# Optimization experiments

Measured on AMD Instinct MI355X. Metric: run time of the kernel, lower is better.

The kernel has to match this reference:

```python
import jax, jax.numpy as jnp
import numpy as np

DIM = 25
N_NODES = 20000
N_EDGES = 320000
NFEAT = 300
NHID = 64
NCLASS = 50


def setup_inputs() -> dict:
    key = jax.random.key(0)
    ks = jax.random.split(key, 8)
    s1 = np.sqrt(6.0 / (NFEAT + NHID))
    s2 = np.sqrt(6.0 / (NHID * DIM + NCLASS))
    return {
        "x": jax.random.normal(ks[0], (N_NODES, NFEAT), dtype=jnp.float32),
        "adj_rows": jax.random.randint(ks[1], (DIM, N_EDGES), 0, N_NODES, dtype=jnp.int32),
        "adj_cols": jax.random.randint(ks[2], (DIM, N_EDGES), 0, N_NODES, dtype=jnp.int32),
        "adj_vals": jax.random.uniform(ks[3], (DIM, N_EDGES), dtype=jnp.float32),
        "W1": jax.random.uniform(ks[4], (DIM, NFEAT, NHID), dtype=jnp.float32, minval=-s1, maxval=s1),
        "b1": jnp.zeros((DIM, NHID), dtype=jnp.float32),
        "W2": jax.random.uniform(ks[5], (DIM, NHID * DIM, NCLASS), dtype=jnp.float32, minval=-s2, maxval=s2),
        "b2": jnp.zeros((DIM, NCLASS), dtype=jnp.float32),
    }


def _spmm(rows, cols, vals, sup, n):
    # sparse [n,n] @ dense [n,f] via gather + segment-sum scatter-add
    return jax.ops.segment_sum(vals[:, None] * sup[cols], rows, num_segments=n)


def reference(x, adj_rows, adj_cols, adj_vals, W1, b1, W2, b2):
    n = x.shape[0]
    spmm = jax.vmap(lambda r, c, v, s: _spmm(r, c, v, s, n))
    # layer 1: per-branch dense mm, spmm, bias, relu  -> [DIM, n, NHID]
    sup1 = jnp.einsum("nf,dfh->dnh", x, W1)
    h1 = jax.nn.relu(spmm(adj_rows, adj_cols, adj_vals, sup1) + b1[:, None, :])
    # permute + reshape: concat branch features per node -> [n, DIM*NHID]
    h1cat = jnp.transpose(h1, (1, 0, 2)).reshape(n, -1)
    # layer 2: per-branch dense mm, spmm, bias, relu -> [DIM, n, NCLASS]
    sup2 = jnp.einsum("nk,dkc->dnc", h1cat, W2)
    h2 = jax.nn.relu(spmm(adj_rows, adj_cols, adj_vals, sup2) + b2[:, None, :])
    # max-pool over branches (POOLING='max')
    return jnp.max(h2, axis=0)
```

## Files before the change

kernel.cpp:

```cpp
#include <hip/hip_runtime.h>
#include <hip/hip_bf16.h>
#include <cstdint>
#include <cstddef>

#define DIM 25
#define NN 20000
#define NE 320000
#define NF 300
#define NH 64
#define NC 50
#define K2 (DIM*NH)
#define KP1 320
#define B1T_ROWS 1664
#define B2T_ROWS 1280
#define NBK 79
#define EPB 4096
#define BPB ((NE + EPB - 1) / EPB)
#define FCAP 5632

typedef __attribute__((ext_vector_type(8))) short short8;
typedef __attribute__((ext_vector_type(4))) float floatx4;
typedef __hip_bfloat16 bf16;

static __device__ __forceinline__ unsigned bf16bits(float f) {
    bf16 b = __float2bfloat16(f);
    return (unsigned)*reinterpret_cast<unsigned short*>(&b);
}
static __device__ __forceinline__ float blo(unsigned w) { return __uint_as_float(w << 16); }
static __device__ __forceinline__ float bhi(unsigned w) { return __uint_as_float(w & 0xFFFF0000u); }

static __device__ __forceinline__ void gld16(const void* g, void* l) {
    __builtin_amdgcn_global_load_lds((const __attribute__((address_space(1))) unsigned*)g,
                                     (__attribute__((address_space(3))) unsigned*)l, 16, 0, 0);
}

__global__ void zero_kernel(int* __restrict__ p, int n) {
    int i = blockIdx.x * blockDim.x + threadIdx.x;
    if (i < n) p[i] = 0;
}

__global__ __launch_bounds__(256) void bucket_scatter_kernel(const int* __restrict__ rows,
                                                             const int* __restrict__ cols,
                                                             const float* __restrict__ vals,
                                                             int* __restrict__ gcur,
                                                             unsigned* __restrict__ interE,
                                                             unsigned char* __restrict__ interR) {
    const int d = blockIdx.y;
    const int e0 = blockIdx.x * EPB;
    __shared__ int lh[NBK];
    __shared__ int lo[NBK];
    __shared__ int lbase[NBK];
    __shared__ unsigned entE[EPB];
    __shared__ unsigned short entR[EPB];
    const int tid = threadIdx.x;
    for (int i = tid; i < NBK; i += 256) lh[i] = 0;
    __syncthreads();
    const int* rd = rows + (size_t)d * NE;
    const int* cd = cols + (size_t)d * NE;
    const float* vd = vals + (size_t)d * NE;
    const int e1 = min(e0 + EPB, NE);
    const int ne = e1 - e0;
    for (int i = e0 + tid; i < e1; i += 256)
        atomicAdd(&lh[rd[i] >> 8], 1);
    __syncthreads();
    if (tid == 0) {
        int run = 0;
        for (int b = 0; b < NBK; ++b) { lo[b] = run; run += lh[b]; }
    }
    __syncthreads();
    for (int i = tid; i < NBK; i += 256) {
        lbase[i] = lh[i] ? atomicAdd(&gcur[d * NBK + i], lh[i]) : 0;
        lh[i] = 0;
    }
    __syncthreads();
    for (int i = e0 + tid; i < e1; i += 256) {
        int r = rd[i];
        int b = r >> 8;
        int rank = atomicAdd(&lh[b], 1);
        int pos = lo[b] + rank;
        entE[pos] = (unsigned)cd[i] | (bf16bits(vd[i]) << 16);
        entR[pos] = (unsigned short)r;
    }
    __syncthreads();
    for (int p = tid; p < ne; p += 256) {
        int r = entR[p];
        int b = r >> 8;
        int gpos = lbase[b] + (p - lo[b]);
        if (gpos < FCAP) {
            size_t slot = ((size_t)d * NBK + b) * FCAP + gpos;
            interE[slot] = entE[p];
            interR[slot] = (unsigned char)r;
        }
    }
}

__global__ void bucket_scan_kernel(const int* __restrict__ gcur,
                                   int* __restrict__ offs_b,
                                   int* __restrict__ bcnt,
                                   int* __restrict__ offs) {
    const int d = blockIdx.x;
    if (threadIdx.x != 0) return;
    int run = 0;
    for (int b = 0; b < NBK; ++b) {
        int c = min(gcur[d * NBK + b], FCAP);
        offs_b[d * NBK + b] = run;
        bcnt[d * NBK + b] = c;
        run += c;
    }
    offs[d * (NN + 1) + NN] = run;
}

__global__ __launch_bounds__(256) void csr_finalize_kernel(const unsigned* __restrict__ interE,
                                                           const unsigned char* __restrict__ interR,
                                                           const int* __restrict__ offs_b,
                                                           const int* __restrict__ bcnt,
                                                           int* __restrict__ offs,
                                                           unsigned* __restrict__ sedge) {
    const int d = blockIdx.y;
    const int b = blockIdx.x;
    const int tid = threadIdx.x;
    const int s = offs_b[d * NBK + b];
    const int cnt = bcnt[d * NBK + b];
    const size_t base = ((size_t)d * NBK + b) * FCAP;
    __shared__ int sm[256];
    __shared__ int cur[256];
    __shared__ unsigned lse[FCAP];
    sm[tid] = 0;
    __syncthreads();
    for (int i = tid; i < cnt; i += 256)
        atomicAdd(&sm[interR[base + i]], 1);
    __syncthreads();
    int own = sm[tid];
    for (int off = 1; off < 256; off <<= 1) {
        int t = (tid >= off) ? sm[tid - off] : 0;
        __syncthreads();
        sm[tid] += t;
        __syncthreads();
    }
    int excl = sm[tid] - own;
    int row = (b << 8) + tid;
    if (row < NN) offs[d * (NN + 1) + row] = s + excl;
    cur[tid] = excl;
    __syncthreads();
    for (int i = tid; i < cnt; i += 256) {
        int idx = atomicAdd(&cur[interR[base + i]], 1);
        lse[idx] = interE[base + i];
    }
    __syncthreads();
    unsigned* sed = sedge + (size_t)d * NE;
    for (int t = tid; t < cnt; t += 256)
        sed[s + t] = lse[t];
}

__global__ void pack_x_kernel(const float* __restrict__ x, bf16* __restrict__ xb) {
    int i = blockIdx.x * blockDim.x + threadIdx.x;
    if (i >= NN * KP1) return;
    int n = i / KP1, k = i - n * KP1;
    xb[i] = __float2bfloat16((k < NF) ? x[(size_t)n * NF + k] : 0.f);
}

__global__ void pack_b1_kernel(const float* __restrict__ W1, bf16* __restrict__ b1t) {
    int i = blockIdx.x * blockDim.x + threadIdx.x;
    if (i >= B1T_ROWS * KP1) return;
    int j2 = i / KP1, k = i - j2 * KP1;
    int chunk = j2 >> 9;
    int r = j2 & 511;
    int d = chunk * 8 + (r >> 6);
    float v = 0.f;
    if (d < DIM && k < NF)
        v = W1[(size_t)d * NF * NH + (size_t)k * NH + (r & 63)];
    b1t[i] = __float2bfloat16(v);
}

__global__ void pack_b2_kernel(const float* __restrict__ W2, bf16* __restrict__ b2t) {
    int i = blockIdx.x * blockDim.x + threadIdx.x;
    if (i >= B2T_ROWS * K2) return;
    int r = i / K2, k = i - r * K2;
    float v = 0.f;
    if (r < DIM * NC) {
        int g = r / NC, c = r - g * NC;
        v = W2[(size_t)g * K2 * NC + (size_t)k * NC + c];
    }
    b2t[i] = __float2bfloat16(v);
}

__global__ __launch_bounds__(256) void gemm_bf16_kernel(const bf16* __restrict__ A, int lda,
                                                        const bf16* __restrict__ BT, int ldb,
                                                        bf16* __restrict__ C,
                                                        int ksteps, int mode, int nvalid) {
    __shared__ unsigned short As[2 * 128 * 32];
    __shared__ unsigned short Bs[2 * 128 * 32];
    const int tid = threadIdx.x;
    const int wave = tid >> 6;
    const int lane = tid & 63;

    const int mtiles = (int)gridDim.x;
    const int ntiles = (int)gridDim.y;
    const int bid = (int)blockIdx.y * mtiles + (int)blockIdx.x;
    const int per_group = 8 * ntiles;
    const int group = bid / per_group;
    const int rem = bid - group * per_group;
    const int first_m = group * 8;
    const int gm = min(8, mtiles - first_m);
    const int mt = first_m + rem % gm;
    const int nt = rem / gm;
    const int m0 = mt * 128;
    const int n0 = nt * 128;

    const int wm = (wave >> 1) * 64;
    const int wn = (wave & 1) * 64;
    floatx4 acc[4][4] = {};
    const int r0 = tid >> 2;
    const int cg = (tid & 3) ^ ((r0 >> 1) & 3);
    const int q8 = (lane >> 4) * 8;
    const int gq = q8 >> 3;
    unsigned short* lA0 = As + wave * 512;
    unsigned short* lA1 = As + 2048 + wave * 512;
    unsigned short* lB0 = Bs + wave * 512;
    unsigned short* lB1 = Bs + 2048 + wave * 512;
    const bf16* gA0 = A + (size_t)(m0 + r0) * lda + cg * 8;
    const bf16* gA1 = A + (size_t)(m0 + r0 + 64) * lda + cg * 8;
    const bf16* gB0 = BT + (size_t)(n0 + r0) * ldb + cg * 8;
    const bf16* gB1 = BT + (size_t)(n0 + r0 + 64) * ldb + cg * 8;

    int offA[4], offB[4];
    #pragma unroll
    for (int i = 0; i < 4; ++i) {
        int ra = wm + i * 16 + (lane & 15);
        int rb = wn + i * 16 + (lane & 15);
        offA[i] = ra * 32 + ((gq ^ ((ra >> 1) & 3)) << 3);
        offB[i] = rb * 32 + ((gq ^ ((rb >> 1) & 3)) << 3);
    }

    gld16(gA0, lA0); gld16(gA1, lA1); gld16(gB0, lB0); gld16(gB1, lB1);
    __syncthreads();

    int cur = 0;
    for (int ks = 0; ks < ksteps; ++ks) {
        if (ks + 1 < ksteps) {
            const int nb = cur ^ 1;
            const size_t ko = (size_t)(ks + 1) * 32;
            gld16(gA0 + ko, lA0 + nb * 4096); gld16(gA1 + ko, lA1 + nb * 4096);
            gld16(gB0 + ko, lB0 + nb * 4096); gld16(gB1 + ko, lB1 + nb * 4096);
        }
        const unsigned short* as = As + cur * 4096;
        const unsigned short* bs = Bs + cur * 4096;
        short8 af[4], bfr[4];
        #pragma unroll
        for (int i = 0; i < 4; ++i) {
            af[i]  = *(const short8*)&as[offA[i]];
            bfr[i] = *(const short8*)&bs[offB[i]];
        }
        #pragma unroll
        for (int i = 0; i < 4; ++i)
            #pragma unroll
            for (int j = 0; j < 4; ++j)
                acc[i][j] = __builtin_amdgcn_mfma_f32_16x16x32_bf16(af[i], bfr[j], acc[i][j], 0, 0, 0);
        __syncthreads();
        cur ^= 1;
    }
    const int cr = (lane >> 4) * 4;
    const int cc = lane & 15;
    #pragma unroll
    for (int i = 0; i < 4; ++i) {
        #pragma unroll
        for (int r = 0; r < 4; ++r) {
            int m = m0 + wm + i * 16 + cr + r;
            if (m >= NN) continue;
            #pragma unroll
            for (int j = 0; j < 4; ++j) {
                int n = n0 + wn + j * 16 + cc;
                if (n >= nvalid) continue;
                if (mode == 1) {
                    int g = n >> 6, h = n & 63;
                    C[(size_t)g * NN * NH + (size_t)m * NH + h] = __float2bfloat16(acc[i][j][r]);
                } else {
                    int g = n / NC, c = n - g * NC;
                    C[(size_t)g * NN * NC + (size_t)m * NC + c] = __float2bfloat16(acc[i][j][r]);
                }
            }
        }
    }
}

__global__ __launch_bounds__(256) void spmm1_kernel(const bf16* __restrict__ sup,
                                                    const int* __restrict__ offs,
                                                    const unsigned* __restrict__ sedge,
                                                    const float* __restrict__ b1,
                                                    bf16* __restrict__ h1cat, int d0, int CHk) {
    const int i = blockIdx.x;
    const int g = i % CHk;
    const int nb = i / CHk;
    const int tid = threadIdx.x;
    const int lane = tid & 63;
    const int n = nb * 8 + ((tid >> 6) << 1) + (lane >> 5);
    const int hl = lane & 31;
    const int d = d0 + g;
    const int s = offs[d * (NN + 1) + n];
    const int e = offs[d * (NN + 1) + n + 1];
    const char* supd = (const char*)sup + (size_t)g * NN * NH * 2;
    const unsigned* sed = sedge + (size_t)d * NE;
    const unsigned hoff = (unsigned)hl * 4;
    float alo0 = 0.f, ahi0 = 0.f, alo1 = 0.f, ahi1 = 0.f;
    int j = s;
    for (; j + 4 <= e; j += 4) {
        unsigned e0 = sed[j], e1 = sed[j + 1], e2 = sed[j + 2], e3 = sed[j + 3];
        unsigned w0 = *(const unsigned*)(supd + (((e0 & 0xFFFFu) << 7) | hoff));
        unsigned w1 = *(const unsigned*)(supd + (((e1 & 0xFFFFu) << 7) | hoff));
        unsigned w2 = *(const unsigned*)(supd + (((e2 & 0xFFFFu) << 7) | hoff));
        unsigned w3 = *(const unsigned*)(supd + (((e3 & 0xFFFFu) << 7) | hoff));
        float v0 = bhi(e0), v1 = bhi(e1), v2 = bhi(e2), v3 = bhi(e3);
        alo0 = fmaf(v0, blo(w0), alo0); ahi0 = fmaf(v0, bhi(w0), ahi0);
        alo1 = fmaf(v1, blo(w1), alo1); ahi1 = fmaf(v1, bhi(w1), ahi1);
        alo0 = fmaf(v2, blo(w2), alo0); ahi0 = fmaf(v2, bhi(w2), ahi0);
        alo1 = fmaf(v3, blo(w3), alo1); ahi1 = fmaf(v3, bhi(w3), ahi1);
    }
    for (; j < e; ++j) {
        unsigned e0 = sed[j];
        unsigned w0 = *(const unsigned*)(supd + (((e0 & 0xFFFFu) << 7) | hoff));
        float v0 = bhi(e0);
        alo0 = fmaf(v0, blo(w0), alo0); ahi0 = fmaf(v0, bhi(w0), ahi0);
    }
    float alo = fmaxf((alo0 + alo1) + b1[d * NH + 2 * hl], 0.f);
    float ahi = fmaxf((ahi0 + ahi1) + b1[d * NH + 2 * hl + 1], 0.f);
    unsigned packed = bf16bits(alo) | (bf16bits(ahi) << 16);
    *(unsigned*)((char*)h1cat + ((size_t)n * K2 + d * NH) * 2 + hoff) = packed;
}

__global__ __launch_bounds__(256) void spmm2b_kernel(const bf16* __restrict__ sup2,
                                                     const int* __restrict__ offs,
                                                     const unsigned* __restrict__ sedge,
                                                     const float* __restrict__ b2,
                                                     unsigned* __restrict__ h2u) {
    const int i = blockIdx.x;
    const int r = i & 7;
    const int q = i >> 3;
    int d, nb;
    if (q < 7500) { d = r + 8 * (q / 2500); nb = q % 2500; }
    else { d = 24; nb = (q - 7500) * 8 + r; if (nb >= 2500) return; }
    const int tid = threadIdx.x;
    const int lane = tid & 63;
    const int n = nb * 8 + ((tid >> 6) << 1) + (lane >> 5);
    const int cl = min(lane & 31, 24);
    const unsigned coff = (unsigned)cl * 4;
    const int s = offs[d * (NN + 1) + n];
    const int e = offs[d * (NN + 1) + n + 1];
    const char* supd = (const char*)sup2 + (size_t)d * NN * NC * 2;
    const unsigned* sed = sedge + (size_t)d * NE;
    float alo0 = b2[d * NC + 2 * cl], ahi0 = b2[d * NC + 2 * cl + 1];
    float alo1 = 0.f, ahi1 = 0.f;
    int j = s;
    for (; j + 4 <= e; j += 4) {
        unsigned e0 = sed[j], e1 = sed[j + 1], e2 = sed[j + 2], e3 = sed[j + 3];
        unsigned w0 = *(const unsigned*)(supd + ((e0 & 0xFFFFu) * 100u + coff));
        unsigned w1 = *(const unsigned*)(supd + ((e1 & 0xFFFFu) * 100u + coff));
        unsigned w2 = *(const unsigned*)(supd + ((e2 & 0xFFFFu) * 100u + coff));
        unsigned w3 = *(const unsigned*)(supd + ((e3 & 0xFFFFu) * 100u + coff));
        float v0 = bhi(e0), v1 = bhi(e1), v2 = bhi(e2), v3 = bhi(e3);
        alo0 = fmaf(v0, blo(w0), alo0); ahi0 = fmaf(v0, bhi(w0), ahi0);
        alo1 = fmaf(v1, blo(w1), alo1); ahi1 = fmaf(v1, bhi(w1), ahi1);
        alo0 = fmaf(v2, blo(w2), alo0); ahi0 = fmaf(v2, bhi(w2), ahi0);
        alo1 = fmaf(v3, blo(w3), alo1); ahi1 = fmaf(v3, bhi(w3), ahi1);
    }
    for (; j < e; ++j) {
        unsigned e0 = sed[j];
        unsigned w0 = *(const unsigned*)(supd + ((e0 & 0xFFFFu) * 100u + coff));
        float v0 = bhi(e0);
        alo0 = fmaf(v0, blo(w0), alo0); ahi0 = fmaf(v0, bhi(w0), ahi0);
    }
    float alo = fmaxf(alo0 + alo1, 0.f);
    float ahi = fmaxf(ahi0 + ahi1, 0.f);
    if ((lane & 31) < 25)
        h2u[((size_t)d * NN + n) * 25 + cl] = bf16bits(alo) | (bf16bits(ahi) << 16);
}

__global__ __launch_bounds__(256) void maxk_kernel(const unsigned* __restrict__ h2u,
                                                   float* __restrict__ out) {
    int i = blockIdx.x * blockDim.x + threadIdx.x;
    if (i >= NN * 25) return;
    int n = i / 25, cl = i - n * 25;
    float mlo = 0.f, mhi = 0.f;
    #pragma unroll
    for (int d = 0; d < DIM; ++d) {
        unsigned w = h2u[(size_t)d * NN * 25 + i];
        mlo = fmaxf(mlo, blo(w));
        mhi = fmaxf(mhi, bhi(w));
    }
    *(float2*)&out[(size_t)n * NC + 2 * cl] = make_float2(mlo, mhi);
}

extern "C" void kernel_launch(void* const* d_in, const int* in_sizes, int n_in,
                              void* d_out, int out_size, void* d_ws, size_t ws_size,
                              hipStream_t stream) {
    const float* x    = (const float*)d_in[0];
    const int*   rows = (const int*)d_in[1];
    const int*   cols = (const int*)d_in[2];
    const float* vals = (const float*)d_in[3];
    const float* W1   = (const float*)d_in[4];
    const float* b1   = (const float*)d_in[5];
    const float* W2   = (const float*)d_in[6];
    const float* b2   = (const float*)d_in[7];
    float* out = (float*)d_out;

    char* ws = (char*)d_ws;
    size_t off = 0;
    auto alloc = [&](size_t bytes) {
        void* p = ws + off;
        off += (bytes + 255) & ~(size_t)255;
        return p;
    };
    bf16* supbuf = (bf16*)alloc(sizeof(bf16) * (size_t)DIM * NN * NC);
    bf16* h1cat  = (bf16*)alloc(sizeof(bf16) * (size_t)NN * K2);
    bf16* b1t    = (bf16*)alloc(sizeof(bf16) * (size_t)B1T_ROWS * KP1);
    bf16* b2t    = (bf16*)alloc(sizeof(bf16) * (size_t)B2T_ROWS * K2);
    int*  offs   = (int*)alloc(sizeof(int) * (size_t)DIM * (NN + 1));
    int*  gcur   = (int*)alloc(sizeof(int) * (size_t)DIM * NBK);
    int*  offs_b = (int*)alloc(sizeof(int) * (size_t)DIM * NBK);
    int*  bcnt   = (int*)alloc(sizeof(int) * (size_t)DIM * NBK);
    unsigned* sedge = (unsigned*)alloc(sizeof(unsigned) * (size_t)DIM * NE);

    bf16* sup1 = supbuf;
    bf16* xbf  = supbuf + (size_t)12 * 1024 * 1024;
    bf16* sup2 = supbuf;
    unsigned* interE = (unsigned*)h1cat;
    unsigned char* interR = (unsigned char*)h1cat + (size_t)DIM * NBK * FCAP * 4;
    unsigned* h2u = (unsigned*)h1cat;

    if (off > ws_size) return;

    zero_kernel<<<(DIM * NBK + 255) / 256, 256, 0, stream>>>(gcur, DIM * NBK);
    bucket_scatter_kernel<<<dim3(BPB, DIM), 256, 0, stream>>>(rows, cols, vals, gcur, interE, interR);
    bucket_scan_kernel<<<DIM, 64, 0, stream>>>(gcur, offs_b, bcnt, offs);
    csr_finalize_kernel<<<dim3(NBK, DIM), 256, 0, stream>>>(interE, interR, offs_b, bcnt, offs, sedge);

    pack_x_kernel<<<(NN * KP1 + 255) / 256, 256, 0, stream>>>(x, xbf);
    pack_b1_kernel<<<(B1T_ROWS * KP1 + 255) / 256, 256, 0, stream>>>(W1, b1t);
    pack_b2_kernel<<<(B2T_ROWS * K2 + 255) / 256, 256, 0, stream>>>(W2, b2t);

    const int mtiles = (NN + 127) / 128;

    const int cstart[4] = {0, 8, 16, 24};
    const int csize[4]  = {8, 8, 8, 1};
    const int crow[4]   = {0, 512, 1024, 1536};
    for (int c = 0; c < 4; ++c) {
        int nv = csize[c] * 64;
        gemm_bf16_kernel<<<dim3(mtiles, (nv + 127) / 128), 256, 0, stream>>>(
            xbf, KP1, b1t + (size_t)crow[c] * KP1, KP1, sup1, KP1 / 32, 1, nv);
        spmm1_kernel<<<csize[c] * (NN / 8), 256, 0, stream>>>(
            sup1, offs, sedge, b1, h1cat, cstart[c], csize[c]);
    }
    gemm_bf16_kernel<<<dim3(mtiles, B2T_ROWS / 128), 256, 0, stream>>>(
        h1cat, K2, b2t, K2, sup2, K2 / 32, 2, DIM * NC);
    spmm2b_kernel<<<8 * 7813, 256, 0, stream>>>(sup2, offs, sedge, b2, h2u);
    maxk_kernel<<<(NN * 25 + 255) / 256, 256, 0, stream>>>(h2u, out);
}
```

Measured before the change: 757.2 us.

## Triple-buffer GEMM LDS tiles with explicit vmcnt waits and single barrier

Moves the bf16 MFMA GEMM from double to triple buffering of A/B tiles in LDS. Loads run two k-steps ahead, and each step uses a partial s_waitcnt vmcnt plus one barrier instead of two __syncthreads. The goal is to hide global-to-LDS load latency and cut barrier stalls. LDS use grows from 32KB to 48KB per block, which may lower occupancy, and the correctness of the inline vmcnt count depends on how gld16 is implemented.

```diff
diff --git a/kernel.cpp b/kernel.cpp
--- a/kernel.cpp
+++ b/kernel.cpp
@@ -188,8 +188,8 @@
                                                         const bf16* __restrict__ BT, int ldb,
                                                         bf16* __restrict__ C,
                                                         int ksteps, int mode, int nvalid) {
-    __shared__ unsigned short As[2 * 128 * 32];
-    __shared__ unsigned short Bs[2 * 128 * 32];
+    __shared__ unsigned short As[3 * 128 * 32];
+    __shared__ unsigned short Bs[3 * 128 * 32];
     const int tid = threadIdx.x;
     const int wave = tid >> 6;
     const int lane = tid & 63;
@@ -233,18 +233,34 @@
     }
 
     gld16(gA0, lA0); gld16(gA1, lA1); gld16(gB0, lB0); gld16(gB1, lB1);
-    __syncthreads();
-
-    int cur = 0;
+    if (ksteps > 1) {
+        gld16(gA0 + 32, lA0 + 4096); gld16(gA1 + 32, lA1 + 4096);
+        gld16(gB0 + 32, lB0 + 4096); gld16(gB1 + 32, lB1 + 4096);
+    }
+    const bf16* pA0 = gA0 + 64;
+    const bf16* pA1 = gA1 + 64;
+    const bf16* pB0 = gB0 + 64;
+    const bf16* pB1 = gB1 + 64;
+
+    int buf = 0;
+    int pbuf = 2;
     for (int ks = 0; ks < ksteps; ++ks) {
-        if (ks + 1 < ksteps) {
-            const int nb = cur ^ 1;
-            const size_t ko = (size_t)(ks + 1) * 32;
-            gld16(gA0 + ko, lA0 + nb * 4096); gld16(gA1 + ko, lA1 + nb * 4096);
-            gld16(gB0 + ko, lB0 + nb * 4096); gld16(gB1 + ko, lB1 + nb * 4096);
+        if (ks + 1 < ksteps) asm volatile("s_waitcnt vmcnt(4)" ::: "memory");
+        else                 asm volatile("s_waitcnt vmcnt(0)" ::: "memory");
+        __builtin_amdgcn_sched_barrier(0);
+        __builtin_amdgcn_s_barrier();
+        __builtin_amdgcn_sched_barrier(0);
+        if (ks + 2 < ksteps) {
+            unsigned short* dA0 = lA0 + pbuf * 4096;
+            unsigned short* dA1 = lA1 + pbuf * 4096;
+            unsigned short* dB0 = lB0 + pbuf * 4096;
+            unsigned short* dB1 = lB1 + pbuf * 4096;
+            gld16(pA0, dA0); gld16(pA1, dA1); gld16(pB0, dB0); gld16(pB1, dB1);
+            pA0 += 32; pA1 += 32; pB0 += 32; pB1 += 32;
+            pbuf = (pbuf == 2) ? 0 : pbuf + 1;
         }
-        const unsigned short* as = As + cur * 4096;
-        const unsigned short* bs = Bs + cur * 4096;
+        const unsigned short* as = As + buf * 4096;
+        const unsigned short* bs = Bs + buf * 4096;
         short8 af[4], bfr[4];
         #pragma unroll
         for (int i = 0; i < 4; ++i) {
@@ -256,8 +272,7 @@
             #pragma unroll
             for (int j = 0; j < 4; ++j)
                 acc[i][j] = __builtin_amdgcn_mfma_f32_16x16x32_bf16(af[i], bfr[j], acc[i][j], 0, 0, 0);
-        __syncthreads();
-        cur ^= 1;
+        buf = (buf == 2) ? 0 : buf + 1;
     }
     const int cr = (lane >> 4) * 4;
     const int cc = lane & 15;
```

Measured after the change: 755.5 us. No clear change (-0.2%).
